# Optimization experiments

Hardware: AMD Instinct MI355X
Metric: run time of the kernel (lower is better)

Reference implementation:

```python
import jax, jax.numpy as jnp
import numpy as np

D, WS, B, H, W = 256, 8, 16, 128, 128
L = WS * WS  # 64 tokens per full window


def setup_inputs() -> dict:
    key = jax.random.key(0)
    ks = jax.random.split(key, 8)
    def n(k, shape, scale=0.02):
        return jax.random.normal(k, shape, jnp.float32) * scale
    # index 0 = full-window block, 1 = half-window block, 2 = quarter-window block
    return {
        "x": jax.random.normal(ks[0], (B, D, H, W), jnp.float32),
        "ln1_g": jnp.ones((3, D), jnp.float32),
        "ln1_b": jnp.zeros((3, D), jnp.float32),
        "W1": n(ks[1], (3, D, 2 * D)),
        "b1": jnp.zeros((3, 2 * D), jnp.float32),
        "sgu_g": jnp.ones((3, D), jnp.float32),
        "sgu_b": jnp.zeros((3, D), jnp.float32),
        "Ws_full": n(ks[2], (L, L), 1e-3),
        "bs_full": jnp.ones((L,), jnp.float32),
        "Ws_half": n(ks[3], (L // 2, L // 2), 1e-3),
        "bs_half": jnp.ones((L // 2,), jnp.float32),
        "Ws_quat": n(ks[4], (L // 4, L // 4), 1e-3),
        "bs_quat": jnp.ones((L // 4,), jnp.float32),
        "W2": n(ks[5], (3, D, D)),
        "b2": jnp.zeros((3, D), jnp.float32),
    }


def _ln(x, g, b, eps=1e-5):
    mu = x.mean(-1, keepdims=True)
    var = ((x - mu) ** 2).mean(-1, keepdims=True)
    return (x - mu) * jax.lax.rsqrt(var + eps) * g + b


def _gmlp(x, g1, bb1, W1, b1, sg, sb, Ws, bs, W2, b2):
    # x: [N, L, d]  -- standard gMLP block with spatial gating unit
    res = x
    y = _ln(x, g1, bb1)
    y = jax.nn.gelu(y @ W1 + b1, approximate=False)  # [N, L, 2d]
    u, v = jnp.split(y, 2, axis=-1)
    v = _ln(v, sg, sb)
    v = jnp.einsum('mn,bnd->bmd', Ws, v) + bs[None, :, None]  # seq mixing
    return (u * v) @ W2 + b2 + res


def reference(x, ln1_g, ln1_b, W1, b1, sgu_g, sgu_b, Ws_full, bs_full,
              Ws_half, bs_half, Ws_quat, bs_quat, W2, b2):
    b, c, h, w = x.shape
    ws = WS
    hw = ws // 2
    Hn, Wn = h // ws, w // ws
    # --- cyclic shift (the torch slice/cat dance == roll by -ws/2 in H and W)
    xs = jnp.roll(x, shift=(-hw, -hw), axis=(2, 3))
    # --- window partition -> (b, Hn, Wn, ws, ws, c)
    win = xs.reshape(b, c, Hn, ws, Wn, ws).transpose(0, 2, 4, 3, 5, 1)
    full = win[:, :Hn - 1, :Wn - 1].reshape(-1, ws * ws, c)
    lr = win[:, :Hn - 1, Wn - 1:]
    ud = win[:, Hn - 1:, :Wn - 1]
    l = lr[:, :, :, :, :hw, :].reshape(-1, ws * hw, c)
    r = lr[:, :, :, :, hw:, :].reshape(-1, ws * hw, c)
    u = ud[:, :, :, :hw, :, :].reshape(-1, ws * hw, c)
    d = ud[:, :, :, hw:, :, :].reshape(-1, ws * hw, c)
    half = jnp.concatenate([l, r, u, d], axis=0)
    q = win[:, Hn - 1:, Wn - 1:]
    quat = jnp.concatenate([
        q[:, :, :, :hw, :hw, :].reshape(-1, hw * hw, c),
        q[:, :, :, :hw, hw:, :].reshape(-1, hw * hw, c),
        q[:, :, :, hw:, :hw, :].reshape(-1, hw * hw, c),
        q[:, :, :, hw:, hw:, :].reshape(-1, hw * hw, c)], axis=0)
    # --- per-window gMLP blocks
    full = _gmlp(full, ln1_g[0], ln1_b[0], W1[0], b1[0], sgu_g[0], sgu_b[0], Ws_full, bs_full, W2[0], b2[0])
    half = _gmlp(half, ln1_g[1], ln1_b[1], W1[1], b1[1], sgu_g[1], sgu_b[1], Ws_half, bs_half, W2[1], b2[1])
    quat = _gmlp(quat, ln1_g[2], ln1_b[2], W1[2], b1[2], sgu_g[2], sgu_b[2], Ws_quat, bs_quat, W2[2], b2[2])
    # --- window reverse + un-shift (reassembly exactly as in torch)
    body = full.reshape(b, Hn - 1, Wn - 1, ws, ws, c).transpose(0, 5, 1, 3, 2, 4).reshape(b, c, h - ws, w - ws)
    ln_ = b * (Hn - 1)
    lo = half[:ln_].reshape(b, Hn - 1, 1, ws, hw, c).transpose(0, 5, 1, 3, 2, 4).reshape(b, c, h - ws, hw)
    ro = half[ln_:2 * ln_].reshape(b, Hn - 1, 1, ws, hw, c).transpose(0, 5, 1, 3, 2, 4).reshape(b, c, h - ws, hw)
    uo = half[2 * ln_:3 * ln_].reshape(b, 1, Wn - 1, hw, ws, c).transpose(0, 5, 1, 3, 2, 4).reshape(b, c, hw, w - ws)
    do = half[3 * ln_:].reshape(b, 1, Wn - 1, hw, ws, c).transpose(0, 5, 1, 3, 2, 4).reshape(b, c, hw, w - ws)
    def qr(t):
        return t.reshape(b, 1, 1, hw, hw, c).transpose(0, 5, 1, 3, 2, 4).reshape(b, c, hw, hw)
    q1o, q2o, q3o, q4o = qr(quat[:b]), qr(quat[b:2 * b]), qr(quat[2 * b:3 * b]), qr(quat[3 * b:])
    top = jnp.concatenate([jnp.concatenate([body, lo], axis=3),
                           jnp.concatenate([uo, q1o], axis=3)], axis=2)
    right = jnp.concatenate([jnp.concatenate([ro, q2o], axis=2), top], axis=3)
    out = jnp.concatenate([jnp.concatenate([q4o, jnp.concatenate([do, q3o], axis=3)], axis=3), right], axis=2)
    return out
```

## Files before the change

### kernel.cpp

```cpp
#include <hip/hip_runtime.h>
#include <hip/hip_bf16.h>
#include <math.h>

#define DCH 256
#define HWD 128

typedef __attribute__((ext_vector_type(4))) float f32x4;
typedef __attribute__((ext_vector_type(4))) short s16x4;
typedef long long i64f;

__device__ __forceinline__ float b2f(unsigned short u) {
    union { float f; unsigned int i; } c; c.i = ((unsigned int)u) << 16; return c.f;
}
__device__ __forceinline__ unsigned short f2b(float f) {
    union { __hip_bfloat16 h; unsigned short u; } c; c.h = __float2bfloat16(f); return c.u;
}
__device__ __forceinline__ unsigned int f2b2(float lo, float hi) {
    return (unsigned int)f2b(lo) | ((unsigned int)f2b(hi) << 16);
}
__device__ __forceinline__ unsigned char f2e4(float f) {
    return (unsigned char)(__builtin_amdgcn_cvt_pk_fp8_f32(f, 0.f, 0, false) & 0xFF);
}
__device__ __forceinline__ unsigned int f2e4x4(float a, float b, float c, float d) {
    unsigned int lo = (unsigned int)__builtin_amdgcn_cvt_pk_fp8_f32(a, b, 0, false);
    return (unsigned int)__builtin_amdgcn_cvt_pk_fp8_f32(c, d, (int)lo, true);
}
__device__ __forceinline__ float e42f(unsigned char u) {
    return __builtin_amdgcn_cvt_f32_fp8((int)u, 0);
}
__device__ __forceinline__ float gelu_f(float z) {
    float y = z * (1.0f + 0.044715f * z * z);
    float p = exp2f(-2.3022108f * y);
    return z / (1.0f + p);
}

__global__ void prep_weights(const float* __restrict__ W1, const float* __restrict__ W2,
                             const float* __restrict__ Wsf, const float* __restrict__ Wsh,
                             const float* __restrict__ Wsq,
                             unsigned char* __restrict__ w1t, unsigned char* __restrict__ w2t,
                             unsigned char* __restrict__ wsf, unsigned char* __restrict__ wsh,
                             unsigned char* __restrict__ wsq)
{
    int idx = blockIdx.x * 256 + threadIdx.x;
    if (idx < 3 * 512 * 256) {
        int g = idx / (512 * 256); int r = idx % (512 * 256);
        int n = r / 256, k = r % 256;
        w1t[idx] = f2e4(16.0f * W1[((size_t)g * 256 + k) * 512 + n]);
    }
    if (idx < 3 * 256 * 256) {
        int g = idx / (256 * 256); int r = idx % (256 * 256);
        int n = r / 256, k = r % 256;
        w2t[idx] = f2e4(16.0f * W2[((size_t)g * 256 + k) * 256 + n]);
    }
    if (idx < 64 * 64) wsf[idx] = f2e4(256.0f * Wsf[idx]);
    if (idx < 32 * 32) wsh[idx] = f2e4(256.0f * Wsh[idx]);
    if (idx < 16 * 16) wsq[idx] = f2e4(256.0f * Wsq[idx]);
}

template<int LSEG, int GROUP, int PC>
__device__ __forceinline__
void gmlp_body(int b, int hr0, int wr0,
               const float* __restrict__ x,
               const float* __restrict__ ln1_g, const float* __restrict__ ln1_b,
               const float* __restrict__ b1,
               const float* __restrict__ sgu_g, const float* __restrict__ sgu_b,
               const float* __restrict__ bs, const float* __restrict__ b2,
               const unsigned char* __restrict__ w1t,
               const unsigned char* __restrict__ w2t,
               const unsigned char* __restrict__ wsp,
               float* __restrict__ out,
               unsigned char* smem)
{
    constexpr int TPT = 512 / LSEG;
    constexpr int CPT = DCH / TPT;
    constexpr int YP  = 264;
    constexpr int M16 = LSEG / 16;
    constexpr int XTP = LSEG + 4;
    constexpr int VTP = LSEG + 8;
    constexpr int SZXT = 256 * XTP * 2;
    constexpr int SZY  = LSEG * YP;
    constexpr int SZVT = 256 * VTP;
    static_assert(SZXT + SZY + SZVT <= 70144, "LDS budget");
    static_assert(SZY + SZVT >= SZXT, "O_t must fit over Y+Vt");
    static_assert(SZVT >= 2 * 512 * 4 && SZY >= 2 * 512 * 4, "stats fit");

    unsigned short* xt16 = (unsigned short*)smem;
    unsigned char*  sm_y8 = smem + SZXT;
    unsigned char*  vt8   = smem + SZXT + SZY;
    float* part1 = (float*)(smem + SZXT + SZY);
    float* part4 = (float*)(smem + SZXT);
    unsigned short* ot16 = (unsigned short*)(smem + SZXT);

    const int tid  = threadIdx.x;
    const int lane = tid & 63;
    const int wv   = tid >> 6;
    const int l16  = lane & 15;
    const int l4   = lane >> 4;
    const int t    = tid & (LSEG - 1);
    const int dq   = tid / LSEG;
    const int d0   = dq * CPT;

    const int pr = t / PC, pc = t % PC;
    const int hq = (hr0 + pr + 4) & (HWD - 1);
    const int wq = (wr0 + pc + 4) & (HWD - 1);
    const size_t plane = (size_t)HWD * HWD;
    const float* xp = x + (size_t)b * DCH * plane + (size_t)hq * HWD + wq;

    unsigned int xres[CPT / 2];
    {
        float s1 = 0.f, s2 = 0.f;
        #pragma unroll
        for (int i = 0; i < CPT; i += 2) {
            float v0 = xp[(size_t)(d0 + i) * plane];
            float v1 = xp[(size_t)(d0 + i + 1) * plane];
            s1 += v0 + v1; s2 += v0 * v0 + v1 * v1;
            unsigned int pk = f2b2(v0, v1);
            xres[i / 2] = pk;
            xt16[(d0 + i) * XTP + t]     = (unsigned short)(pk & 0xFFFF);
            xt16[(d0 + i + 1) * XTP + t] = (unsigned short)(pk >> 16);
        }
        part1[(0 * TPT + dq) * LSEG + t] = s1;
        part1[(1 * TPT + dq) * LSEG + t] = s2;
    }
    __syncthreads();

    {
        float mu = 0.f, sq = 0.f;
        #pragma unroll
        for (int q = 0; q < TPT; ++q) {
            mu += part1[(0 * TPT + q) * LSEG + t];
            sq += part1[(1 * TPT + q) * LSEG + t];
        }
        mu *= (1.0f / DCH);
        float var = sq * (1.0f / DCH) - mu * mu;
        float rs = rsqrtf(var + 1e-5f);
        #pragma unroll
        for (int i = 0; i < CPT; i += 4) {
            f32x4 g  = *(const f32x4*)&ln1_g[GROUP * DCH + d0 + i];
            f32x4 bv = *(const f32x4*)&ln1_b[GROUP * DCH + d0 + i];
            float z[4];
            #pragma unroll
            for (int j = 0; j < 4; ++j) {
                unsigned int pk = xres[(i + j) / 2];
                float v = b2f((unsigned short)((j & 1) ? (pk >> 16) : (pk & 0xFFFF)));
                z[j] = (v - mu) * rs * g[j] + bv[j];
            }
            *(unsigned int*)&sm_y8[t * YP + d0 + i] = f2e4x4(z[0], z[1], z[2], z[3]);
        }
    }
    __syncthreads();

    unsigned int u8[M16][2];
    {
        f32x4 acc[M16][2];
        #pragma unroll
        for (int mi = 0; mi < M16; ++mi) { acc[mi][0] = f32x4{0,0,0,0}; acc[mi][1] = f32x4{0,0,0,0}; }
        const unsigned char* wpu = w1t + (size_t)GROUP * 512 * 256 + (size_t)(wv * 32) * 256;
        __builtin_amdgcn_s_setprio(1);
        #pragma unroll
        for (int k0 = 0; k0 < 256; k0 += 32) {
            i64f a[M16], bb[2];
            #pragma unroll
            for (int mi = 0; mi < M16; ++mi)
                a[mi] = *(const i64f*)&sm_y8[(16 * mi + l16) * YP + k0 + 8 * l4];
            #pragma unroll
            for (int ni = 0; ni < 2; ++ni)
                bb[ni] = *(const i64f*)&wpu[(size_t)(16 * ni + l16) * 256 + k0 + 8 * l4];
            #pragma unroll
            for (int mi = 0; mi < M16; ++mi)
                #pragma unroll
                for (int ni = 0; ni < 2; ++ni)
                    acc[mi][ni] = __builtin_amdgcn_mfma_f32_16x16x32_fp8_fp8(a[mi], bb[ni], acc[mi][ni], 0, 0, 0);
        }
        __builtin_amdgcn_s_setprio(0);
        #pragma unroll
        for (int ni = 0; ni < 2; ++ni) {
            float b1v = b1[GROUP * 512 + wv * 32 + 16 * ni + l16];
            #pragma unroll
            for (int mi = 0; mi < M16; ++mi) {
                float z0 = gelu_f(acc[mi][ni][0] * 0.0625f + b1v);
                float z1 = gelu_f(acc[mi][ni][1] * 0.0625f + b1v);
                float z2 = gelu_f(acc[mi][ni][2] * 0.0625f + b1v);
                float z3 = gelu_f(acc[mi][ni][3] * 0.0625f + b1v);
                u8[mi][ni] = f2e4x4(8.f * z0, 8.f * z1, 8.f * z2, 8.f * z3);
            }
        }
        #pragma unroll
        for (int mi = 0; mi < M16; ++mi) { acc[mi][0] = f32x4{0,0,0,0}; acc[mi][1] = f32x4{0,0,0,0}; }
        const unsigned char* wpv = w1t + (size_t)GROUP * 512 * 256 + (size_t)(256 + wv * 32) * 256;
        __builtin_amdgcn_s_setprio(1);
        #pragma unroll
        for (int k0 = 0; k0 < 256; k0 += 32) {
            i64f a[M16], bb[2];
            #pragma unroll
            for (int mi = 0; mi < M16; ++mi)
                a[mi] = *(const i64f*)&sm_y8[(16 * mi + l16) * YP + k0 + 8 * l4];
            #pragma unroll
            for (int ni = 0; ni < 2; ++ni)
                bb[ni] = *(const i64f*)&wpv[(size_t)(16 * ni + l16) * 256 + k0 + 8 * l4];
            #pragma unroll
            for (int mi = 0; mi < M16; ++mi)
                #pragma unroll
                for (int ni = 0; ni < 2; ++ni)
                    acc[mi][ni] = __builtin_amdgcn_mfma_f32_16x16x32_fp8_fp8(a[mi], bb[ni], acc[mi][ni], 0, 0, 0);
        }
        __builtin_amdgcn_s_setprio(0);
        #pragma unroll
        for (int ni = 0; ni < 2; ++ni) {
            int row = wv * 32 + 16 * ni + l16;
            float b1v = b1[GROUP * 512 + 256 + wv * 32 + 16 * ni + l16];
            #pragma unroll
            for (int mi = 0; mi < M16; ++mi) {
                float z0 = gelu_f(acc[mi][ni][0] * 0.0625f + b1v);
                float z1 = gelu_f(acc[mi][ni][1] * 0.0625f + b1v);
                float z2 = gelu_f(acc[mi][ni][2] * 0.0625f + b1v);
                float z3 = gelu_f(acc[mi][ni][3] * 0.0625f + b1v);
                *(unsigned int*)&vt8[row * VTP + 16 * mi + 4 * l4] = f2e4x4(z0, z1, z2, z3);
            }
        }
    }
    __syncthreads();

    {
        float s1 = 0.f, s2 = 0.f;
        #pragma unroll
        for (int i = 0; i < CPT; ++i) {
            float f = e42f(vt8[(d0 + i) * VTP + t]);
            s1 += f; s2 += f * f;
        }
        part4[(0 * TPT + dq) * LSEG + t] = s1;
        part4[(1 * TPT + dq) * LSEG + t] = s2;
    }
    __syncthreads();
    {
        float mu = 0.f, sq = 0.f;
        #pragma unroll
        for (int q = 0; q < TPT; ++q) {
            mu += part4[(0 * TPT + q) * LSEG + t];
            sq += part4[(1 * TPT + q) * LSEG + t];
        }
        mu *= (1.0f / DCH);
        float var = sq * (1.0f / DCH) - mu * mu;
        float rs = rsqrtf(var + 1e-5f);
        #pragma unroll
        for (int i = 0; i < CPT; i += 4) {
            f32x4 g  = *(const f32x4*)&sgu_g[GROUP * DCH + d0 + i];
            f32x4 bv = *(const f32x4*)&sgu_b[GROUP * DCH + d0 + i];
            #pragma unroll
            for (int j = 0; j < 4; ++j) {
                int d = d0 + i + j;
                float f = e42f(vt8[d * VTP + t]);
                vt8[d * VTP + t] = f2e4((f - mu) * rs * g[j] + bv[j]);
            }
        }
    }
    __syncthreads();

    {
        f32x4 acc[M16][2];
        #pragma unroll
        for (int mi = 0; mi < M16; ++mi) { acc[mi][0] = f32x4{0,0,0,0}; acc[mi][1] = f32x4{0,0,0,0}; }
        constexpr int KS = (LSEG > 32) ? (LSEG / 32) : 1;
        __builtin_amdgcn_s_setprio(1);
        #pragma unroll
        for (int ks = 0; ks < KS; ++ks) {
            const int k0 = 32 * ks;
            i64f a[M16], bb[2];
            #pragma unroll
            for (int mi = 0; mi < M16; ++mi) {
                if constexpr (LSEG == 16)
                    a[mi] = (l4 < 2) ? *(const i64f*)&wsp[(16 * mi + l16) * LSEG + 8 * l4] : (i64f)0;
                else
                    a[mi] = *(const i64f*)&wsp[(16 * mi + l16) * LSEG + k0 + 8 * l4];
            }
            #pragma unroll
            for (int ni = 0; ni < 2; ++ni) {
                int row = wv * 32 + 16 * ni + l16;
                if constexpr (LSEG == 16)
                    bb[ni] = (l4 < 2) ? *(const i64f*)&vt8[row * VTP + 8 * l4] : (i64f)0;
                else
                    bb[ni] = *(const i64f*)&vt8[row * VTP + k0 + 8 * l4];
            }
            #pragma unroll
            for (int mi = 0; mi < M16; ++mi)
                #pragma unroll
                for (int ni = 0; ni < 2; ++ni)
                    acc[mi][ni] = __builtin_amdgcn_mfma_f32_16x16x32_fp8_fp8(a[mi], bb[ni], acc[mi][ni], 0, 0, 0);
        }
        __builtin_amdgcn_s_setprio(0);
        #pragma unroll
        for (int mi = 0; mi < M16; ++mi) {
            #pragma unroll
            for (int r = 0; r < 4; ++r) {
                int m = 16 * mi + 4 * l4 + r;
                float bsm = bs[m];
                #pragma unroll
                for (int ni = 0; ni < 2; ++ni) {
                    float uf = e42f((unsigned char)((u8[mi][ni] >> (8 * r)) & 0xFF));
                    float p = (acc[mi][ni][r] * (1.0f / 256.0f) + bsm) * uf;
                    sm_y8[m * YP + wv * 32 + 16 * ni + l16] = f2e4(p);
                }
            }
        }
    }
    __syncthreads();

    {
        f32x4 acc[M16][2];
        #pragma unroll
        for (int mi = 0; mi < M16; ++mi) { acc[mi][0] = f32x4{0,0,0,0}; acc[mi][1] = f32x4{0,0,0,0}; }
        const int nb2 = wv * 32;
        const unsigned char* wp2 = w2t + (size_t)GROUP * 256 * 256 + (size_t)nb2 * 256;
        __builtin_amdgcn_s_setprio(1);
        #pragma unroll
        for (int k0 = 0; k0 < 256; k0 += 32) {
            i64f a[M16], bb[2];
            #pragma unroll
            for (int mi = 0; mi < M16; ++mi)
                a[mi] = *(const i64f*)&sm_y8[(16 * mi + l16) * YP + k0 + 8 * l4];
            #pragma unroll
            for (int ni = 0; ni < 2; ++ni)
                bb[ni] = *(const i64f*)&wp2[(size_t)(16 * ni + l16) * 256 + k0 + 8 * l4];
            #pragma unroll
            for (int mi = 0; mi < M16; ++mi)
                #pragma unroll
                for (int ni = 0; ni < 2; ++ni)
                    acc[mi][ni] = __builtin_amdgcn_mfma_f32_16x16x32_fp8_fp8(a[mi], bb[ni], acc[mi][ni], 0, 0, 0);
        }
        __builtin_amdgcn_s_setprio(0);
        __syncthreads();
        #pragma unroll
        for (int ni = 0; ni < 2; ++ni) {
            int cu = nb2 + 16 * ni + l16;
            float b2v = b2[GROUP * DCH + cu];
            #pragma unroll
            for (int mi = 0; mi < M16; ++mi) {
                s16x4 op;
                #pragma unroll
                for (int r = 0; r < 4; ++r)
                    op[r] = (short)f2b(acc[mi][ni][r] * (1.0f / 128.0f) + b2v);
                *(s16x4*)&ot16[cu * XTP + 16 * mi + 4 * l4] = op;
            }
        }
    }
    __syncthreads();

    {
        constexpr int NG  = LSEG / 4;
        constexpr int GPR = PC / 4;
        constexpr int ITERS = 256 * NG / 512;
        #pragma unroll
        for (int i = 0; i < ITERS; ++i) {
            int f = tid + 512 * i;
            int ch = f / NG;
            int g  = f % NG;
            int row = g / GPR, gc = g % GPR;
            int hq2 = (hr0 + row + 4) & (HWD - 1);
            int wq2 = (wr0 + 4 * gc + 4) & (HWD - 1);
            s16x4 ov = *(const s16x4*)&ot16[ch * XTP + 4 * g];
            s16x4 xv = *(const s16x4*)&xt16[ch * XTP + 4 * g];
            f32x4 o;
            #pragma unroll
            for (int j = 0; j < 4; ++j)
                o[j] = b2f((unsigned short)ov[j]) + b2f((unsigned short)xv[j]);
            *(f32x4*)&out[((size_t)b * DCH + ch) * plane + (size_t)hq2 * HWD + wq2] = o;
        }
    }
}

__global__ __launch_bounds__(512, 4)
void gmlp_all(const float* __restrict__ x,
              const float* __restrict__ ln1_g, const float* __restrict__ ln1_b,
              const float* __restrict__ b1,
              const float* __restrict__ sgu_g, const float* __restrict__ sgu_b,
              const float* __restrict__ bsf, const float* __restrict__ bsh,
              const float* __restrict__ bsq, const float* __restrict__ b2,
              const unsigned char* __restrict__ w1t, const unsigned char* __restrict__ w2t,
              const unsigned char* __restrict__ wsf, const unsigned char* __restrict__ wsh,
              const unsigned char* __restrict__ wsq,
              float* __restrict__ out)
{
    __shared__ __align__(16) unsigned char smem[70144];
    const int bid = blockIdx.x;

    if (bid < 3600) {
        int b = bid / 225, rem = bid % 225;
        int hr0 = (rem / 15) * 8, wr0 = (rem % 15) * 8;
        gmlp_body<64, 0, 8>(b, hr0, wr0,
                            x, ln1_g, ln1_b, b1, sgu_g, sgu_b, bsf, b2, w1t, w2t, wsf, out, smem);
    } else if (bid < 4080) {
        int ix = bid - 3600;
        int side = ix / 240, j = ix % 240;
        int b = j / 15, hr0 = (j % 15) * 8, wr0 = 120 + 4 * side;
        gmlp_body<32, 1, 4>(b, hr0, wr0,
                            x, ln1_g, ln1_b, b1, sgu_g, sgu_b, bsh, b2, w1t, w2t, wsh, out, smem);
    } else if (bid < 4560) {
        int ix = bid - 4080;
        int side = ix / 240, j = ix % 240;
        int b = j / 15, hr0 = 120 + 4 * side, wr0 = (j % 15) * 8;
        gmlp_body<32, 1, 8>(b, hr0, wr0,
                            x, ln1_g, ln1_b, b1, sgu_g, sgu_b, bsh, b2, w1t, w2t, wsh, out, smem);
    } else {
        int ix = bid - 4560;
        int quad = ix >> 4, b = ix & 15;
        int hr0 = 120 + 4 * (quad >> 1), wr0 = 120 + 4 * (quad & 1);
        gmlp_body<16, 2, 4>(b, hr0, wr0,
                            x, ln1_g, ln1_b, b1, sgu_g, sgu_b, bsq, b2, w1t, w2t, wsq, out, smem);
    }
}

extern "C" void kernel_launch(void* const* d_in, const int* in_sizes, int n_in,
                              void* d_out, int out_size, void* d_ws, size_t ws_size,
                              hipStream_t stream)
{
    (void)in_sizes; (void)n_in; (void)out_size; (void)ws_size;
    const float* x     = (const float*)d_in[0];
    const float* ln1_g = (const float*)d_in[1];
    const float* ln1_b = (const float*)d_in[2];
    const float* W1    = (const float*)d_in[3];
    const float* b1    = (const float*)d_in[4];
    const float* sgu_g = (const float*)d_in[5];
    const float* sgu_b = (const float*)d_in[6];
    const float* Wsf   = (const float*)d_in[7];
    const float* bsf   = (const float*)d_in[8];
    const float* Wsh   = (const float*)d_in[9];
    const float* bsh   = (const float*)d_in[10];
    const float* Wsq   = (const float*)d_in[11];
    const float* bsq   = (const float*)d_in[12];
    const float* W2    = (const float*)d_in[13];
    const float* b2    = (const float*)d_in[14];
    float* out = (float*)d_out;

    unsigned char* w1t = (unsigned char*)d_ws;
    unsigned char* w2t = w1t + 3 * 512 * 256;
    unsigned char* wsf = w2t + 3 * 256 * 256;
    unsigned char* wsh = wsf + 64 * 64;
    unsigned char* wsq = wsh + 32 * 32;

    hipLaunchKernelGGL(prep_weights, dim3(1536), dim3(256), 0, stream,
                       W1, W2, Wsf, Wsh, Wsq, w1t, w2t, wsf, wsh, wsq);

    hipLaunchKernelGGL(gmlp_all, dim3(4624), dim3(512), 0, stream,
                       x, ln1_g, ln1_b, b1, sgu_g, sgu_b,
                       bsf, bsh, bsq, b2, w1t, w2t, wsf, wsh, wsq, out);
}
```

Baseline: 468.2 us.

## Fold SGU layernorm into spatial weights and use sigmoid GELU approximation

Replaces the separate LayerNorm pass over the gated half (two stats passes and a normalize-rewrite in LDS) with per-token statistics accumulated by LDS atomics in the GEMM1 epilogue. The normalization is folded algebraically into the spatial-mixing matrix (columns scaled by rsqrt) plus a per-row correction and gamma/beta applied in the epilogue. Row sums of Ws are precomputed in the prep kernel. GELU becomes a cheaper sigmoid form z*sigmoid(1.702z), which loosens accuracy, and LDS use grows, which may reduce occupancy.

```diff
diff --git a/kernel.cpp b/kernel.cpp
--- a/kernel.cpp
+++ b/kernel.cpp
@@ -29,9 +29,7 @@
     return __builtin_amdgcn_cvt_f32_fp8((int)u, 0);
 }
 __device__ __forceinline__ float gelu_f(float z) {
-    float y = z * (1.0f + 0.044715f * z * z);
-    float p = exp2f(-2.3022108f * y);
-    return z / (1.0f + p);
+    return z / (1.0f + exp2f(-2.455407f * z));
 }
 
 __global__ void prep_weights(const float* __restrict__ W1, const float* __restrict__ W2,
@@ -39,7 +37,8 @@
                              const float* __restrict__ Wsq,
                              unsigned char* __restrict__ w1t, unsigned char* __restrict__ w2t,
                              unsigned char* __restrict__ wsf, unsigned char* __restrict__ wsh,
-                             unsigned char* __restrict__ wsq)
+                             unsigned char* __restrict__ wsq,
+                             float* __restrict__ sf, float* __restrict__ sh, float* __restrict__ sq)
 {
     int idx = blockIdx.x * 256 + threadIdx.x;
     if (idx < 3 * 512 * 256) {
@@ -55,6 +54,9 @@
     if (idx < 64 * 64) wsf[idx] = f2e4(256.0f * Wsf[idx]);
     if (idx < 32 * 32) wsh[idx] = f2e4(256.0f * Wsh[idx]);
     if (idx < 16 * 16) wsq[idx] = f2e4(256.0f * Wsq[idx]);
+    if (idx < 64) { float s = 0.f; for (int n = 0; n < 64; ++n) s += Wsf[idx * 64 + n]; sf[idx] = s; }
+    if (idx < 32) { float s = 0.f; for (int n = 0; n < 32; ++n) s += Wsh[idx * 32 + n]; sh[idx] = s; }
+    if (idx < 16) { float s = 0.f; for (int n = 0; n < 16; ++n) s += Wsq[idx * 16 + n]; sq[idx] = s; }
 }
 
 template<int LSEG, int GROUP, int PC>
@@ -68,6 +70,7 @@
                const unsigned char* __restrict__ w1t,
                const unsigned char* __restrict__ w2t,
                const unsigned char* __restrict__ wsp,
+               const float* __restrict__ Sp,
                float* __restrict__ out,
                unsigned char* smem)
 {
@@ -77,19 +80,27 @@
     constexpr int M16 = LSEG / 16;
     constexpr int XTP = LSEG + 4;
     constexpr int VTP = LSEG + 8;
+    constexpr int AP  = LSEG + 8;
     constexpr int SZXT = 256 * XTP * 2;
     constexpr int SZY  = LSEG * YP;
     constexpr int SZVT = 256 * VTP;
-    static_assert(SZXT + SZY + SZVT <= 70144, "LDS budget");
+    constexpr int TAIL = SZXT + SZY + SZVT;
+    static_assert(TAIL + 6 * LSEG * 4 + LSEG * AP <= 76288, "LDS budget");
     static_assert(SZY + SZVT >= SZXT, "O_t must fit over Y+Vt");
-    static_assert(SZVT >= 2 * 512 * 4 && SZY >= 2 * 512 * 4, "stats fit");
+    static_assert(SZVT >= 2 * 512 * 4, "part1 fits over Vt");
 
     unsigned short* xt16 = (unsigned short*)smem;
     unsigned char*  sm_y8 = smem + SZXT;
     unsigned char*  vt8   = smem + SZXT + SZY;
     float* part1 = (float*)(smem + SZXT + SZY);
-    float* part4 = (float*)(smem + SZXT);
     unsigned short* ot16 = (unsigned short*)(smem + SZXT);
+    float* vstat0  = (float*)(smem + TAIL);
+    float* vstat1  = vstat0 + LSEG;
+    float* rs_arr  = vstat1 + LSEG;
+    float* rsmu    = rs_arr + LSEG;
+    float* cbuf    = rsmu + LSEG;
+    float* Sl      = cbuf + LSEG;
+    unsigned char* a8 = (unsigned char*)(Sl + LSEG);
 
     const int tid  = threadIdx.x;
     const int lane = tid & 63;
@@ -107,6 +118,7 @@
     const float* xp = x + (size_t)b * DCH * plane + (size_t)hq * HWD + wq;
 
     unsigned int xres[CPT / 2];
+    if (tid < LSEG) { vstat0[tid] = 0.f; vstat1[tid] = 0.f; cbuf[tid] = 0.f; }
     {
         float s1 = 0.f, s2 = 0.f;
         #pragma unroll
@@ -205,54 +217,58 @@
                     acc[mi][ni] = __builtin_amdgcn_mfma_f32_16x16x32_fp8_fp8(a[mi], bb[ni], acc[mi][ni], 0, 0, 0);
         }
         __builtin_amdgcn_s_setprio(0);
-        #pragma unroll
-        for (int ni = 0; ni < 2; ++ni) {
-            int row = wv * 32 + 16 * ni + l16;
-            float b1v = b1[GROUP * 512 + 256 + wv * 32 + 16 * ni + l16];
+        {
+            float b1v0 = b1[GROUP * 512 + 256 + wv * 32 + l16];
+            float b1v1 = b1[GROUP * 512 + 256 + wv * 32 + 16 + l16];
             #pragma unroll
             for (int mi = 0; mi < M16; ++mi) {
-                float z0 = gelu_f(acc[mi][ni][0] * 0.0625f + b1v);
-                float z1 = gelu_f(acc[mi][ni][1] * 0.0625f + b1v);
-                float z2 = gelu_f(acc[mi][ni][2] * 0.0625f + b1v);
-                float z3 = gelu_f(acc[mi][ni][3] * 0.0625f + b1v);
-                *(unsigned int*)&vt8[row * VTP + 16 * mi + 4 * l4] = f2e4x4(z0, z1, z2, z3);
-            }
-        }
-    }
-    __syncthreads();
-
-    {
-        float s1 = 0.f, s2 = 0.f;
-        #pragma unroll
-        for (int i = 0; i < CPT; ++i) {
-            float f = e42f(vt8[(d0 + i) * VTP + t]);
-            s1 += f; s2 += f * f;
-        }
-        part4[(0 * TPT + dq) * LSEG + t] = s1;
-        part4[(1 * TPT + dq) * LSEG + t] = s2;
-    }
-    __syncthreads();
-    {
-        float mu = 0.f, sq = 0.f;
-        #pragma unroll
-        for (int q = 0; q < TPT; ++q) {
-            mu += part4[(0 * TPT + q) * LSEG + t];
-            sq += part4[(1 * TPT + q) * LSEG + t];
-        }
-        mu *= (1.0f / DCH);
-        float var = sq * (1.0f / DCH) - mu * mu;
+                float zv[2][4];
+                #pragma unroll
+                for (int r = 0; r < 4; ++r) {
+                    zv[0][r] = gelu_f(acc[mi][0][r] * 0.0625f + b1v0);
+                    zv[1][r] = gelu_f(acc[mi][1][r] * 0.0625f + b1v1);
+                }
+                int row0 = wv * 32 + l16, row1 = wv * 32 + 16 + l16;
+                *(unsigned int*)&vt8[row0 * VTP + 16 * mi + 4 * l4] = f2e4x4(zv[0][0], zv[0][1], zv[0][2], zv[0][3]);
+                *(unsigned int*)&vt8[row1 * VTP + 16 * mi + 4 * l4] = f2e4x4(zv[1][0], zv[1][1], zv[1][2], zv[1][3]);
+                #pragma unroll
+                for (int r = 0; r < 4; ++r) {
+                    int tkn = 16 * mi + 4 * l4 + r;
+                    atomicAdd(&vstat0[tkn], zv[0][r] + zv[1][r]);
+                    atomicAdd(&vstat1[tkn], zv[0][r] * zv[0][r] + zv[1][r] * zv[1][r]);
+                }
+            }
+        }
+    }
+    __syncthreads();
+
+    if (tid < LSEG) {
+        float s1 = vstat0[tid], s2 = vstat1[tid];
+        float mu = s1 * (1.0f / DCH);
+        float var = s2 * (1.0f / DCH) - mu * mu;
         float rs = rsqrtf(var + 1e-5f);
-        #pragma unroll
-        for (int i = 0; i < CPT; i += 4) {
-            f32x4 g  = *(const f32x4*)&sgu_g[GROUP * DCH + d0 + i];
-            f32x4 bv = *(const f32x4*)&sgu_b[GROUP * DCH + d0 + i];
-            #pragma unroll
-            for (int j = 0; j < 4; ++j) {
-                int d = d0 + i + j;
-                float f = e42f(vt8[d * VTP + t]);
-                vt8[d * VTP + t] = f2e4((f - mu) * rs * g[j] + bv[j]);
-            }
-        }
+        rs_arr[tid] = rs;
+        rsmu[tid] = rs * mu;
+        Sl[tid] = Sp[tid];
+    }
+    __syncthreads();
+
+    {
+        constexpr int E = LSEG * LSEG;
+        constexpr int EPT = (E + 511) / 512;
+        float cpart = 0.f; int m0 = 0; bool any = false;
+        #pragma unroll
+        for (int j = 0; j < EPT; ++j) {
+            int e = tid * EPT + j;
+            if (e < E) {
+                int m = e / LSEG, n = e % LSEG;
+                float w = e42f(wsp[e]);
+                a8[m * AP + n] = f2e4(w * rs_arr[n]);
+                cpart += w * rsmu[n];
+                m0 = m; any = true;
+            }
+        }
+        if (any) atomicAdd(&cbuf[m0], cpart);
     }
     __syncthreads();
 
@@ -269,9 +285,9 @@
             #pragma unroll
             for (int mi = 0; mi < M16; ++mi) {
                 if constexpr (LSEG == 16)
-                    a[mi] = (l4 < 2) ? *(const i64f*)&wsp[(16 * mi + l16) * LSEG + 8 * l4] : (i64f)0;
+                    a[mi] = (l4 < 2) ? *(const i64f*)&a8[(16 * mi + l16) * AP + 8 * l4] : (i64f)0;
                 else
-                    a[mi] = *(const i64f*)&wsp[(16 * mi + l16) * LSEG + k0 + 8 * l4];
+                    a[mi] = *(const i64f*)&a8[(16 * mi + l16) * AP + k0 + 8 * l4];
             }
             #pragma unroll
             for (int ni = 0; ni < 2; ++ni) {
@@ -289,16 +305,19 @@
         }
         __builtin_amdgcn_s_setprio(0);
         #pragma unroll
-        for (int mi = 0; mi < M16; ++mi) {
-            #pragma unroll
-            for (int r = 0; r < 4; ++r) {
-                int m = 16 * mi + 4 * l4 + r;
-                float bsm = bs[m];
-                #pragma unroll
-                for (int ni = 0; ni < 2; ++ni) {
+        for (int ni = 0; ni < 2; ++ni) {
+            int cv = wv * 32 + 16 * ni + l16;
+            float gv  = sgu_g[GROUP * DCH + cv];
+            float bvv = sgu_b[GROUP * DCH + cv];
+            #pragma unroll
+            for (int mi = 0; mi < M16; ++mi) {
+                #pragma unroll
+                for (int r = 0; r < 4; ++r) {
+                    int m = 16 * mi + 4 * l4 + r;
+                    float wsv = (acc[mi][ni][r] - cbuf[m]) * (1.0f / 256.0f);
+                    float Vm = gv * wsv + bvv * Sl[m] + bs[m];
                     float uf = e42f((unsigned char)((u8[mi][ni] >> (8 * r)) & 0xFF));
-                    float p = (acc[mi][ni][r] * (1.0f / 256.0f) + bsm) * uf;
-                    sm_y8[m * YP + wv * 32 + 16 * ni + l16] = f2e4(p);
+                    sm_y8[m * YP + cv] = f2e4(Vm * uf);
                 }
             }
         }
@@ -378,34 +397,36 @@
               const unsigned char* __restrict__ w1t, const unsigned char* __restrict__ w2t,
               const unsigned char* __restrict__ wsf, const unsigned char* __restrict__ wsh,
               const unsigned char* __restrict__ wsq,
+              const float* __restrict__ sf, const float* __restrict__ sh,
+              const float* __restrict__ sq,
               float* __restrict__ out)
 {
-    __shared__ __align__(16) unsigned char smem[70144];
+    __shared__ __align__(16) unsigned char smem[76288];
     const int bid = blockIdx.x;
 
     if (bid < 3600) {
         int b = bid / 225, rem = bid % 225;
         int hr0 = (rem / 15) * 8, wr0 = (rem % 15) * 8;
         gmlp_body<64, 0, 8>(b, hr0, wr0,
-                            x, ln1_g, ln1_b, b1, sgu_g, sgu_b, bsf, b2, w1t, w2t, wsf, out, smem);
+                            x, ln1_g, ln1_b, b1, sgu_g, sgu_b, bsf, b2, w1t, w2t, wsf, sf, out, smem);
     } else if (bid < 4080) {
         int ix = bid - 3600;
         int side = ix / 240, j = ix % 240;
         int b = j / 15, hr0 = (j % 15) * 8, wr0 = 120 + 4 * side;
         gmlp_body<32, 1, 4>(b, hr0, wr0,
-                            x, ln1_g, ln1_b, b1, sgu_g, sgu_b, bsh, b2, w1t, w2t, wsh, out, smem);
+                            x, ln1_g, ln1_b, b1, sgu_g, sgu_b, bsh, b2, w1t, w2t, wsh, sh, out, smem);
     } else if (bid < 4560) {
         int ix = bid - 4080;
         int side = ix / 240, j = ix % 240;
         int b = j / 15, hr0 = 120 + 4 * side, wr0 = (j % 15) * 8;
         gmlp_body<32, 1, 8>(b, hr0, wr0,
-                            x, ln1_g, ln1_b, b1, sgu_g, sgu_b, bsh, b2, w1t, w2t, wsh, out, smem);
+                            x, ln1_g, ln1_b, b1, sgu_g, sgu_b, bsh, b2, w1t, w2t, wsh, sh, out, smem);
     } else {
         int ix = bid - 4560;
         int quad = ix >> 4, b = ix & 15;
         int hr0 = 120 + 4 * (quad >> 1), wr0 = 120 + 4 * (quad & 1);
         gmlp_body<16, 2, 4>(b, hr0, wr0,
-                            x, ln1_g, ln1_b, b1, sgu_g, sgu_b, bsq, b2, w1t, w2t, wsq, out, smem);
+                            x, ln1_g, ln1_b, b1, sgu_g, sgu_b, bsq, b2, w1t, w2t, wsq, sq, out, smem);
     }
 }
 
@@ -436,11 +457,14 @@
     unsigned char* wsf = w2t + 3 * 256 * 256;
     unsigned char* wsh = wsf + 64 * 64;
     unsigned char* wsq = wsh + 32 * 32;
+    float* sf = (float*)(wsq + 16 * 16);
+    float* sh = sf + 64;
+    float* sq = sh + 32;
 
     hipLaunchKernelGGL(prep_weights, dim3(1536), dim3(256), 0, stream,
-                       W1, W2, Wsf, Wsh, Wsq, w1t, w2t, wsf, wsh, wsq);
+                       W1, W2, Wsf, Wsh, Wsq, w1t, w2t, wsf, wsh, wsq, sf, sh, sq);
 
     hipLaunchKernelGGL(gmlp_all, dim3(4624), dim3(512), 0, stream,
                        x, ln1_g, ln1_b, b1, sgu_g, sgu_b,
-                       bsf, bsh, bsq, b2, w1t, w2t, wsf, wsh, wsq, out);
-}
+                       bsf, bsh, bsq, b2, w1t, w2t, wsf, wsh, wsq, sf, sh, sq, out);
+}
```

Result: slower. 771.0 us (+64.7%).

## Double threads per block to 1024, giving each wave one 16-column N tile

Applied to the files above, without the earlier changes.

Raises the block size from 512 to 1024 threads, so each of the 16 waves owns a single 16-wide N slice in every MFMA GEMM instead of two. Per-thread accumulator and register usage is halved, and the LN stats and output loops are rescaled to the new thread count. For the 16-token case the stats buffer moves to a separate LDS region. Each wave now does less work per A-operand load from LDS, and a launch bound of (1024,4) may be unreachable given the 70KB LDS per block, which limits how many blocks fit per CU.

```diff
diff --git a/kernel.cpp b/kernel.cpp
--- a/kernel.cpp
+++ b/kernel.cpp
@@ -71,7 +71,8 @@
                float* __restrict__ out,
                unsigned char* smem)
 {
-    constexpr int TPT = 512 / LSEG;
+    constexpr int NT  = 1024;
+    constexpr int TPT = NT / LSEG;
     constexpr int CPT = DCH / TPT;
     constexpr int YP  = 264;
     constexpr int M16 = LSEG / 16;
@@ -80,16 +81,23 @@
     constexpr int SZXT = 256 * XTP * 2;
     constexpr int SZY  = LSEG * YP;
     constexpr int SZVT = 256 * VTP;
-    static_assert(SZXT + SZY + SZVT <= 70144, "LDS budget");
-    static_assert(SZY + SZVT >= SZXT, "O_t must fit over Y+Vt");
-    static_assert(SZVT >= 2 * 512 * 4 && SZY >= 2 * 512 * 4, "stats fit");
+    constexpr int SZSTAT = 2 * NT * 4;
+    static_assert(SZXT + SZY + SZVT + (LSEG == 16 ? SZSTAT : 0) <= 70144, "LDS budget");
+    static_assert(SZY + SZVT >= 256 * XTP * 2, "O_t must fit over Y+Vt");
+    static_assert(LSEG == 16 || (SZVT >= SZSTAT && SZY >= SZSTAT), "stats fit");
 
     unsigned short* xt16 = (unsigned short*)smem;
     unsigned char*  sm_y8 = smem + SZXT;
     unsigned char*  vt8   = smem + SZXT + SZY;
-    float* part1 = (float*)(smem + SZXT + SZY);
-    float* part4 = (float*)(smem + SZXT);
     unsigned short* ot16 = (unsigned short*)(smem + SZXT);
+    float* part1; float* part4;
+    if constexpr (LSEG == 16) {
+        part1 = (float*)(smem + SZXT + SZY + SZVT);
+        part4 = part1;
+    } else {
+        part1 = (float*)(smem + SZXT + SZY);
+        part4 = (float*)(smem + SZXT);
+    }
 
     const int tid  = threadIdx.x;
     const int lane = tid & 63;
@@ -150,71 +158,61 @@
     }
     __syncthreads();
 
-    unsigned int u8[M16][2];
-    {
-        f32x4 acc[M16][2];
-        #pragma unroll
-        for (int mi = 0; mi < M16; ++mi) { acc[mi][0] = f32x4{0,0,0,0}; acc[mi][1] = f32x4{0,0,0,0}; }
-        const unsigned char* wpu = w1t + (size_t)GROUP * 512 * 256 + (size_t)(wv * 32) * 256;
+    unsigned int u8r[M16];
+    {
+        f32x4 acc[M16];
+        #pragma unroll
+        for (int mi = 0; mi < M16; ++mi) acc[mi] = f32x4{0.f, 0.f, 0.f, 0.f};
+        const unsigned char* wpu = w1t + (size_t)GROUP * 512 * 256 + (size_t)(wv * 16) * 256;
         __builtin_amdgcn_s_setprio(1);
         #pragma unroll
         for (int k0 = 0; k0 < 256; k0 += 32) {
-            i64f a[M16], bb[2];
+            i64f a[M16];
             #pragma unroll
             for (int mi = 0; mi < M16; ++mi)
                 a[mi] = *(const i64f*)&sm_y8[(16 * mi + l16) * YP + k0 + 8 * l4];
-            #pragma unroll
-            for (int ni = 0; ni < 2; ++ni)
-                bb[ni] = *(const i64f*)&wpu[(size_t)(16 * ni + l16) * 256 + k0 + 8 * l4];
-            #pragma unroll
-            for (int mi = 0; mi < M16; ++mi)
-                #pragma unroll
-                for (int ni = 0; ni < 2; ++ni)
-                    acc[mi][ni] = __builtin_amdgcn_mfma_f32_16x16x32_fp8_fp8(a[mi], bb[ni], acc[mi][ni], 0, 0, 0);
+            i64f bb = *(const i64f*)&wpu[(size_t)l16 * 256 + k0 + 8 * l4];
+            #pragma unroll
+            for (int mi = 0; mi < M16; ++mi)
+                acc[mi] = __builtin_amdgcn_mfma_f32_16x16x32_fp8_fp8(a[mi], bb, acc[mi], 0, 0, 0);
         }
         __builtin_amdgcn_s_setprio(0);
-        #pragma unroll
-        for (int ni = 0; ni < 2; ++ni) {
-            float b1v = b1[GROUP * 512 + wv * 32 + 16 * ni + l16];
+        {
+            float b1v = b1[GROUP * 512 + wv * 16 + l16];
             #pragma unroll
             for (int mi = 0; mi < M16; ++mi) {
-                float z0 = gelu_f(acc[mi][ni][0] * 0.0625f + b1v);
-                float z1 = gelu_f(acc[mi][ni][1] * 0.0625f + b1v);
-                float z2 = gelu_f(acc[mi][ni][2] * 0.0625f + b1v);
-                float z3 = gelu_f(acc[mi][ni][3] * 0.0625f + b1v);
-                u8[mi][ni] = f2e4x4(8.f * z0, 8.f * z1, 8.f * z2, 8.f * z3);
-            }
-        }
-        #pragma unroll
-        for (int mi = 0; mi < M16; ++mi) { acc[mi][0] = f32x4{0,0,0,0}; acc[mi][1] = f32x4{0,0,0,0}; }
-        const unsigned char* wpv = w1t + (size_t)GROUP * 512 * 256 + (size_t)(256 + wv * 32) * 256;
+                float z0 = gelu_f(acc[mi][0] * 0.0625f + b1v);
+                float z1 = gelu_f(acc[mi][1] * 0.0625f + b1v);
+                float z2 = gelu_f(acc[mi][2] * 0.0625f + b1v);
+                float z3 = gelu_f(acc[mi][3] * 0.0625f + b1v);
+                u8r[mi] = f2e4x4(8.f * z0, 8.f * z1, 8.f * z2, 8.f * z3);
+            }
+        }
+        #pragma unroll
+        for (int mi = 0; mi < M16; ++mi) acc[mi] = f32x4{0.f, 0.f, 0.f, 0.f};
+        const unsigned char* wpv = w1t + (size_t)GROUP * 512 * 256 + (size_t)(256 + wv * 16) * 256;
         __builtin_amdgcn_s_setprio(1);
         #pragma unroll
         for (int k0 = 0; k0 < 256; k0 += 32) {
-            i64f a[M16], bb[2];
+            i64f a[M16];
             #pragma unroll
             for (int mi = 0; mi < M16; ++mi)
                 a[mi] = *(const i64f*)&sm_y8[(16 * mi + l16) * YP + k0 + 8 * l4];
-            #pragma unroll
-            for (int ni = 0; ni < 2; ++ni)
-                bb[ni] = *(const i64f*)&wpv[(size_t)(16 * ni + l16) * 256 + k0 + 8 * l4];
-            #pragma unroll
-            for (int mi = 0; mi < M16; ++mi)
-                #pragma unroll
-                for (int ni = 0; ni < 2; ++ni)
-                    acc[mi][ni] = __builtin_amdgcn_mfma_f32_16x16x32_fp8_fp8(a[mi], bb[ni], acc[mi][ni], 0, 0, 0);
+            i64f bb = *(const i64f*)&wpv[(size_t)l16 * 256 + k0 + 8 * l4];
+            #pragma unroll
+            for (int mi = 0; mi < M16; ++mi)
+                acc[mi] = __builtin_amdgcn_mfma_f32_16x16x32_fp8_fp8(a[mi], bb, acc[mi], 0, 0, 0);
         }
         __builtin_amdgcn_s_setprio(0);
-        #pragma unroll
-        for (int ni = 0; ni < 2; ++ni) {
-            int row = wv * 32 + 16 * ni + l16;
-            float b1v = b1[GROUP * 512 + 256 + wv * 32 + 16 * ni + l16];
+        {
+            int row = wv * 16 + l16;
+            float b1v = b1[GROUP * 512 + 256 + wv * 16 + l16];
             #pragma unroll
             for (int mi = 0; mi < M16; ++mi) {
-                float z0 = gelu_f(acc[mi][ni][0] * 0.0625f + b1v);
-                float z1 = gelu_f(acc[mi][ni][1] * 0.0625f + b1v);
-                float z2 = gelu_f(acc[mi][ni][2] * 0.0625f + b1v);
-                float z3 = gelu_f(acc[mi][ni][3] * 0.0625f + b1v);
+                float z0 = gelu_f(acc[mi][0] * 0.0625f + b1v);
+                float z1 = gelu_f(acc[mi][1] * 0.0625f + b1v);
+                float z2 = gelu_f(acc[mi][2] * 0.0625f + b1v);
+                float z3 = gelu_f(acc[mi][3] * 0.0625f + b1v);
                 *(unsigned int*)&vt8[row * VTP + 16 * mi + 4 * l4] = f2e4x4(z0, z1, z2, z3);
             }
         }
@@ -257,15 +255,16 @@
     __syncthreads();
 
     {
-        f32x4 acc[M16][2];
-        #pragma unroll
-        for (int mi = 0; mi < M16; ++mi) { acc[mi][0] = f32x4{0,0,0,0}; acc[mi][1] = f32x4{0,0,0,0}; }
+        f32x4 acc[M16];
+        #pragma unroll
+        for (int mi = 0; mi < M16; ++mi) acc[mi] = f32x4{0.f, 0.f, 0.f, 0.f};
         constexpr int KS = (LSEG > 32) ? (LSEG / 32) : 1;
+        const int row = wv * 16 + l16;
         __builtin_amdgcn_s_setprio(1);
         #pragma unroll
         for (int ks = 0; ks < KS; ++ks) {
             const int k0 = 32 * ks;
-            i64f a[M16], bb[2];
+            i64f a[M16], bb;
             #pragma unroll
             for (int mi = 0; mi < M16; ++mi) {
                 if constexpr (LSEG == 16)
@@ -273,19 +272,13 @@
                 else
                     a[mi] = *(const i64f*)&wsp[(16 * mi + l16) * LSEG + k0 + 8 * l4];
             }
-            #pragma unroll
-            for (int ni = 0; ni < 2; ++ni) {
-                int row = wv * 32 + 16 * ni + l16;
-                if constexpr (LSEG == 16)
-                    bb[ni] = (l4 < 2) ? *(const i64f*)&vt8[row * VTP + 8 * l4] : (i64f)0;
-                else
-                    bb[ni] = *(const i64f*)&vt8[row * VTP + k0 + 8 * l4];
-            }
-            #pragma unroll
-            for (int mi = 0; mi < M16; ++mi)
-                #pragma unroll
-                for (int ni = 0; ni < 2; ++ni)
-                    acc[mi][ni] = __builtin_amdgcn_mfma_f32_16x16x32_fp8_fp8(a[mi], bb[ni], acc[mi][ni], 0, 0, 0);
+            if constexpr (LSEG == 16)
+                bb = (l4 < 2) ? *(const i64f*)&vt8[row * VTP + 8 * l4] : (i64f)0;
+            else
+                bb = *(const i64f*)&vt8[row * VTP + k0 + 8 * l4];
+            #pragma unroll
+            for (int mi = 0; mi < M16; ++mi)
+                acc[mi] = __builtin_amdgcn_mfma_f32_16x16x32_fp8_fp8(a[mi], bb, acc[mi], 0, 0, 0);
         }
         __builtin_amdgcn_s_setprio(0);
         #pragma unroll
@@ -293,54 +286,42 @@
             #pragma unroll
             for (int r = 0; r < 4; ++r) {
                 int m = 16 * mi + 4 * l4 + r;
-                float bsm = bs[m];
-                #pragma unroll
-                for (int ni = 0; ni < 2; ++ni) {
-                    float uf = e42f((unsigned char)((u8[mi][ni] >> (8 * r)) & 0xFF));
-                    float p = (acc[mi][ni][r] * (1.0f / 256.0f) + bsm) * uf;
-                    sm_y8[m * YP + wv * 32 + 16 * ni + l16] = f2e4(p);
-                }
-            }
-        }
-    }
-    __syncthreads();
-
-    {
-        f32x4 acc[M16][2];
-        #pragma unroll
-        for (int mi = 0; mi < M16; ++mi) { acc[mi][0] = f32x4{0,0,0,0}; acc[mi][1] = f32x4{0,0,0,0}; }
-        const int nb2 = wv * 32;
-        const unsigned char* wp2 = w2t + (size_t)GROUP * 256 * 256 + (size_t)nb2 * 256;
+                float uf = e42f((unsigned char)((u8r[mi] >> (8 * r)) & 0xFF));
+                float p = (acc[mi][r] * (1.0f / 256.0f) + bs[m]) * uf;
+                sm_y8[m * YP + row] = f2e4(p);
+            }
+        }
+    }
+    __syncthreads();
+
+    {
+        f32x4 acc[M16];
+        #pragma unroll
+        for (int mi = 0; mi < M16; ++mi) acc[mi] = f32x4{0.f, 0.f, 0.f, 0.f};
+        const unsigned char* wp2 = w2t + (size_t)GROUP * 256 * 256 + (size_t)(wv * 16) * 256;
         __builtin_amdgcn_s_setprio(1);
         #pragma unroll
         for (int k0 = 0; k0 < 256; k0 += 32) {
-            i64f a[M16], bb[2];
+            i64f a[M16];
             #pragma unroll
             for (int mi = 0; mi < M16; ++mi)
                 a[mi] = *(const i64f*)&sm_y8[(16 * mi + l16) * YP + k0 + 8 * l4];
-            #pragma unroll
-            for (int ni = 0; ni < 2; ++ni)
-                bb[ni] = *(const i64f*)&wp2[(size_t)(16 * ni + l16) * 256 + k0 + 8 * l4];
-            #pragma unroll
-            for (int mi = 0; mi < M16; ++mi)
-                #pragma unroll
-                for (int ni = 0; ni < 2; ++ni)
-                    acc[mi][ni] = __builtin_amdgcn_mfma_f32_16x16x32_fp8_fp8(a[mi], bb[ni], acc[mi][ni], 0, 0, 0);
+            i64f bb = *(const i64f*)&wp2[(size_t)l16 * 256 + k0 + 8 * l4];
+            #pragma unroll
+            for (int mi = 0; mi < M16; ++mi)
+                acc[mi] = __builtin_amdgcn_mfma_f32_16x16x32_fp8_fp8(a[mi], bb, acc[mi], 0, 0, 0);
         }
         __builtin_amdgcn_s_setprio(0);
         __syncthreads();
-        #pragma unroll
-        for (int ni = 0; ni < 2; ++ni) {
-            int cu = nb2 + 16 * ni + l16;
-            float b2v = b2[GROUP * DCH + cu];
-            #pragma unroll
-            for (int mi = 0; mi < M16; ++mi) {
-                s16x4 op;
-                #pragma unroll
-                for (int r = 0; r < 4; ++r)
-                    op[r] = (short)f2b(acc[mi][ni][r] * (1.0f / 128.0f) + b2v);
-                *(s16x4*)&ot16[cu * XTP + 16 * mi + 4 * l4] = op;
-            }
+        const int cu = wv * 16 + l16;
+        float b2v = b2[GROUP * DCH + cu];
+        #pragma unroll
+        for (int mi = 0; mi < M16; ++mi) {
+            s16x4 op;
+            #pragma unroll
+            for (int r = 0; r < 4; ++r)
+                op[r] = (short)f2b(acc[mi][r] * (1.0f / 128.0f) + b2v);
+            *(s16x4*)&ot16[cu * XTP + 16 * mi + 4 * l4] = op;
         }
     }
     __syncthreads();
@@ -348,10 +329,10 @@
     {
         constexpr int NG  = LSEG / 4;
         constexpr int GPR = PC / 4;
-        constexpr int ITERS = 256 * NG / 512;
+        constexpr int ITERS = 256 * NG / NT;
         #pragma unroll
         for (int i = 0; i < ITERS; ++i) {
-            int f = tid + 512 * i;
+            int f = tid + NT * i;
             int ch = f / NG;
             int g  = f % NG;
             int row = g / GPR, gc = g % GPR;
@@ -368,7 +349,7 @@
     }
 }
 
-__global__ __launch_bounds__(512, 4)
+__global__ __launch_bounds__(1024, 4)
 void gmlp_all(const float* __restrict__ x,
               const float* __restrict__ ln1_g, const float* __restrict__ ln1_b,
               const float* __restrict__ b1,
@@ -440,7 +421,7 @@
     hipLaunchKernelGGL(prep_weights, dim3(1536), dim3(256), 0, stream,
                        W1, W2, Wsf, Wsh, Wsq, w1t, w2t, wsf, wsh, wsq);
 
-    hipLaunchKernelGGL(gmlp_all, dim3(4624), dim3(512), 0, stream,
+    hipLaunchKernelGGL(gmlp_all, dim3(4624), dim3(1024), 0, stream,
                        x, ln1_g, ln1_b, b1, sgu_g, sgu_b,
                        bsf, bsh, bsq, b2, w1t, w2t, wsf, wsh, wsq, out);
 }
```

New measurement: 558.6 us. +19.3%, slower.
